# Kernel tuning notes

Measured on AMD Instinct MI355X. Metric: run time of the kernel, lower is better.

Reference implementation:

```python
import jax, jax.numpy as jnp
import numpy as np

NUM_NODES = 16384
NUM_EDGES = 131072
NUM_MOLS = 512
H = 256          # hidden_dim
L = 3            # num_hidden_layers
NUM_RBF = 50
CUTOFF = 5.0
IN_DIM = 5
D_IN = IN_DIM + 3  # atom_types + spherical coords


def setup_inputs() -> dict:
    ks = jax.random.split(jax.random.key(0), 32)
    n = lambda k, s: jax.random.normal(k, s, dtype=jnp.float32) * 0.05
    return {
        "atom_types": jax.random.uniform(ks[0], (NUM_NODES, IN_DIM), dtype=jnp.float32),
        "coords_spherical": jax.random.normal(ks[1], (NUM_NODES, 3), dtype=jnp.float32),
        "edge_dist": jax.random.uniform(ks[2], (NUM_EDGES,), dtype=jnp.float32) * CUTOFF,
        "edge_index": jax.random.randint(ks[3], (2, NUM_EDGES), 0, NUM_NODES, dtype=jnp.int32),
        "node2mol": jnp.arange(NUM_NODES, dtype=jnp.int32) // (NUM_NODES // NUM_MOLS),
        "emb_Wm": n(ks[4], (D_IN, H)), "emb_bm": jnp.zeros((H,), jnp.float32),
        "emb_Wp": n(ks[5], (D_IN, H)), "emb_bp": jnp.zeros((H,), jnp.float32),
        "attn_Wqm": n(ks[6], (L, H, H)), "attn_Wkm": n(ks[7], (L, H, H)), "attn_Wvm": n(ks[8], (L, H, H)),
        "attn_Wqp": n(ks[9], (L, H, H)), "attn_Wkp": n(ks[10], (L, H, H)), "attn_Wvp": n(ks[11], (L, H, H)),
        "attn_We": n(ks[12], (L, NUM_RBF)), "attn_be": jnp.zeros((L,), jnp.float32),
        "mp_We": n(ks[13], (L, NUM_RBF, H)), "mp_be": jnp.zeros((L, H), jnp.float32),
        "mp_Wm": n(ks[14], (L, H, H)), "mp_bm": jnp.zeros((L, H), jnp.float32),
        "mp_Wp": n(ks[15], (L, H, H)), "mp_bp": jnp.zeros((L, H), jnp.float32),
        "ln_g": jnp.ones((L, H), jnp.float32), "ln_b": jnp.zeros((L, H), jnp.float32),
        "proj_W": n(ks[16], (H, H)), "proj_b": jnp.zeros((H,), jnp.float32),
        "head_W1": n(ks[17], (2 * H, H)), "head_b1": jnp.zeros((H,), jnp.float32),
        "head_W2": n(ks[18], (H, H // 2)), "head_b2": jnp.zeros((H // 2,), jnp.float32),
        "head_W3": n(ks[19], (H // 2, 1)), "head_b3": jnp.zeros((1,), jnp.float32),
    }


def _seg_softmax(s, seg, n):
    m = jax.ops.segment_max(s, seg, num_segments=n)
    e = jnp.exp(s - m[seg])
    z = jax.ops.segment_sum(e, seg, num_segments=n)
    return e / (z[seg] + 1e-9)


def _layernorm(x, g, b):
    mu = x.mean(-1, keepdims=True)
    v = ((x - mu) ** 2).mean(-1, keepdims=True)
    return (x - mu) * jax.lax.rsqrt(v + 1e-5) * g + b


def _forward(atom_types, coords_spherical, edge_dist,
             emb_Wm, emb_bm, emb_Wp, emb_bp,
             attn_Wqm, attn_Wkm, attn_Wvm, attn_Wqp, attn_Wkp, attn_Wvp, attn_We, attn_be,
             mp_We, mp_be, mp_Wm, mp_bm, mp_Wp, mp_bp,
             ln_g, ln_b, proj_W, proj_b,
             head_W1, head_b1, head_W2, head_b2, head_W3, head_b3,
             edge_index, node2mol):
    src, dst = edge_index[0], edge_index[1]
    N = NUM_NODES

    # --- RBF expansion (Schutt 2018): 50 gaussians on [0, cutoff] * cosine cutoff ---
    centers = jnp.linspace(0.0, CUTOFF, NUM_RBF)
    delta = CUTOFF / NUM_RBF
    env = 0.5 * (jnp.cos(jnp.pi * edge_dist / CUTOFF) + 1.0) * (edge_dist < CUTOFF)
    rbf = jnp.exp(-0.5 * ((edge_dist[:, None] - centers) / delta) ** 2) * env[:, None]  # [E, R]

    # --- Complex polar embedding ---
    x = jnp.concatenate([atom_types, coords_spherical], axis=-1)  # [N, 8]
    mag = jax.nn.softplus(x @ emb_Wm + emb_bm)
    ph = jnp.pi * jnp.tanh(x @ emb_Wp + emb_bp)

    for l in range(L):
        # --- Complex polar attention: |q||k| cos(phi_q - phi_k), edge bias from rbf ---
        qm, km, vm = mag @ attn_Wqm[l], mag @ attn_Wkm[l], mag @ attn_Wvm[l]
        qp, kp, vp = ph @ attn_Wqp[l], ph @ attn_Wkp[l], ph @ attn_Wvp[l]
        score = jnp.sum(qm[dst] * km[src] * jnp.cos(qp[dst] - kp[src]), axis=-1) / jnp.sqrt(float(H))
        score = score + rbf @ attn_We[l] + attn_be[l]          # [E]
        alpha = _seg_softmax(score, dst, N)                    # [E]
        new_mag = jax.ops.segment_sum(alpha[:, None] * vm[src], dst, num_segments=N)
        new_ph = jax.ops.segment_sum(alpha[:, None] * vp[src], dst, num_segments=N)

        # --- Complex message passing gated by RBF profile ---
        gate = jax.nn.silu(rbf @ mp_We[l] + mp_be[l])          # [E, H]
        agg_m = jax.ops.segment_sum(gate * new_mag[src], dst, num_segments=N)
        agg_p = jax.ops.segment_sum(gate * new_ph[src], dst, num_segments=N)
        new_mag = new_mag + agg_m @ mp_Wm[l] + mp_bm[l]
        new_ph = new_ph + agg_p @ mp_Wp[l] + mp_bp[l]

        # --- residual + LayerNorm on magnitude (dropout = identity at eval) ---
        new_mag = new_mag + mag
        new_ph = new_ph + ph
        mag = _layernorm(new_mag, ln_g[l], ln_b[l])
        ph = new_ph

    # --- real projection + dual (mean, sum) pooling per molecule ---
    atom_repr = (mag * jnp.cos(ph)) @ proj_W + proj_b          # [N, H]
    s = jax.ops.segment_sum(atom_repr, node2mol, num_segments=NUM_MOLS)
    cnt = jax.ops.segment_sum(jnp.ones((N, 1), atom_repr.dtype), node2mol, num_segments=NUM_MOLS)
    mol = jnp.concatenate([s / jnp.maximum(cnt, 1.0), s], axis=-1)  # [B, 2H]

    h = jax.nn.silu(mol @ head_W1 + head_b1)
    h = jax.nn.silu(h @ head_W2 + head_b2)
    return h @ head_W3 + head_b3                               # [B, 1]


def reference(atom_types, coords_spherical, edge_dist,
              emb_Wm, emb_bm, emb_Wp, emb_bp,
              attn_Wqm, attn_Wkm, attn_Wvm, attn_Wqp, attn_Wkp, attn_Wvp, attn_We, attn_be,
              mp_We, mp_be, mp_Wm, mp_bm, mp_Wp, mp_bp,
              ln_g, ln_b, proj_W, proj_b,
              head_W1, head_b1, head_W2, head_b2, head_W3, head_b3,
              edge_index, node2mol):
    return _forward(atom_types, coords_spherical, edge_dist,
                    emb_Wm, emb_bm, emb_Wp, emb_bp,
                    attn_Wqm, attn_Wkm, attn_Wvm, attn_Wqp, attn_Wkp, attn_Wvp, attn_We, attn_be,
                    mp_We, mp_be, mp_Wm, mp_bm, mp_Wp, mp_bp,
                    ln_g, ln_b, proj_W, proj_b,
                    head_W1, head_b1, head_W2, head_b2, head_W3, head_b3,
                    edge_index, node2mol)
```

## Files before the change

### kernel.cpp

```cpp
#include <hip/hip_runtime.h>
#include <math.h>

#define N_NODES 16384
#define N_EDGES 131072
#define N_MOLS 512
#define HDIM 256
#define NLAYER 3
#define NRBF 50
#define CUT 5.0f
#define HH (HDIM*HDIM)

typedef unsigned short u16;
typedef __attribute__((ext_vector_type(8))) short short8v;
typedef __attribute__((ext_vector_type(4))) float f32x4;
typedef __attribute__((ext_vector_type(4))) unsigned short u16x4;

__device__ __forceinline__ float softplusf(float x){ return fmaxf(x,0.f)+log1pf(expf(-fabsf(x))); }
__device__ __forceinline__ float siluf(float x){ return x/(1.f+expf(-x)); }
__device__ __forceinline__ float bf2f(u16 u){ union{unsigned int i; float f;}v; v.i=((unsigned int)u)<<16; return v.f; }
__device__ __forceinline__ u16 f2bf(float f){ union{float f; unsigned int i;}v; v.f=f; unsigned int r = v.i + 0x7FFFu + ((v.i>>16)&1u); return (u16)(r>>16); }

__device__ __forceinline__ void gload_lds16(const void* g, void* l){
  __builtin_amdgcn_global_load_lds((const __attribute__((address_space(1))) unsigned int*)g,
                                   (__attribute__((address_space(3))) unsigned int*)l, 16, 0, 0);
}

__global__ void k_hist(const int* __restrict__ dst, int* __restrict__ cnt){
  int e = blockIdx.x*256 + threadIdx.x;
  if(e < N_EDGES) atomicAdd(&cnt[dst[e]], 1);
}

__global__ __launch_bounds__(1024) void k_scan(const int* __restrict__ cnt,
                                               int* __restrict__ rowptr,
                                               int* __restrict__ cursor){
  __shared__ int part[1024];
  int tid = threadIdx.x;
  int base = tid*16;
  int loc[16]; int s=0;
  #pragma unroll
  for(int i=0;i<16;i++){ loc[i]=s; s+=cnt[base+i]; }
  part[tid]=s; __syncthreads();
  for(int off=1; off<1024; off<<=1){
    int v = (tid>=off)? part[tid-off] : 0;
    __syncthreads();
    part[tid] += v;
    __syncthreads();
  }
  int pre = (tid==0)?0:part[tid-1];
  #pragma unroll
  for(int i=0;i<16;i++){ int v = pre+loc[i]; rowptr[base+i]=v; cursor[base+i]=v; }
  if(tid==1023) rowptr[N_NODES]=part[1023];
}

__global__ void k_scatter(const int* __restrict__ dst, int* __restrict__ cursor,
                          int* __restrict__ perm){
  int e = blockIdx.x*256+threadIdx.x;
  if(e<N_EDGES){ int p = atomicAdd(&cursor[dst[e]],1); perm[p]=e; }
}

__global__ void k_rbf(const float* __restrict__ dist, u16* __restrict__ rbf){
  int gid = blockIdx.x*256+threadIdx.x;
  int e = gid>>6, r = gid&63;
  u16 o = 0;
  if(r<NRBF){
    float d = dist[e];
    float env = 0.5f*(cosf(3.14159265358979f*d/CUT)+1.f) * (d<CUT ? 1.f:0.f);
    float c = CUT*(float)r/(float)(NRBF-1);
    float u = (d - c)/(CUT/(float)NRBF);
    o = f2bf(expf(-0.5f*u*u)*env);
  }
  rbf[(size_t)e*64+r] = o;
}

struct WDesc { const float* src; u16* dst; int K; int dK; };
struct WArgs { WDesc d[28]; };
__global__ __launch_bounds__(256) void k_wconv(WArgs a){
  WDesc w = a.d[blockIdx.x];
  int t = blockIdx.y;
  int ky = t >> 3, nx = t & 7;
  if(ky*32 >= w.dK) return;
  __shared__ float tile[32][33];
  int tid = threadIdx.x;
  int kk = tid >> 3, n4 = (tid & 7)*4;
  int k = ky*32 + kk;
  float4 v = {0.f,0.f,0.f,0.f};
  if(k < w.K) v = *(const float4*)(w.src + (size_t)k*HDIM + nx*32 + n4);
  tile[kk][n4+0]=v.x; tile[kk][n4+1]=v.y; tile[kk][n4+2]=v.z; tile[kk][n4+3]=v.w;
  __syncthreads();
  int nn = tid >> 3, k4 = (tid & 7)*4;
  u16x4 o;
  #pragma unroll
  for(int j=0;j<4;j++) o[j] = f2bf(tile[k4+j][nn]);
  *(u16x4*)(w.dst + (size_t)(nx*32+nn)*w.dK + ky*32 + k4) = o;
}

__global__ void k_embed(const float* __restrict__ at, const float* __restrict__ co,
                        const float* __restrict__ Wm, const float* __restrict__ bm,
                        const float* __restrict__ Wp, const float* __restrict__ bp,
                        float* __restrict__ mag, float* __restrict__ ph,
                        u16* __restrict__ magb, u16* __restrict__ phb){
  int n = blockIdx.x; int h = threadIdx.x;
  __shared__ float x[8];
  if(threadIdx.x<5) x[threadIdx.x] = at[n*5+threadIdx.x];
  else if(threadIdx.x<8) x[threadIdx.x] = co[n*3+threadIdx.x-5];
  __syncthreads();
  float tm=bm[h], tp=bp[h];
  #pragma unroll
  for(int i=0;i<8;i++){ tm = fmaf(x[i],Wm[i*HDIM+h],tm); tp = fmaf(x[i],Wp[i*HDIM+h],tp); }
  size_t idx = (size_t)n*HDIM+h;
  float m = softplusf(tm);
  float p = 3.14159265358979f*tanhf(tp);
  mag[idx]=m; ph[idx]=p; magb[idx]=f2bf(m); phb[idx]=f2bf(p);
}

template<int MODE>
__device__ __forceinline__ void gemm_body(const u16* __restrict__ A,
                                          const u16* __restrict__ Bt,
                                          const float* __restrict__ bias,
                                          void* __restrict__ outp, int K){
  __shared__ __align__(16) u16 As[128*64];
  __shared__ __align__(16) u16 Bs[64*64];
  int tid = threadIdx.x;
  int lane = tid & 63, wid = tid >> 6;
  int wm = wid & 1, wn = wid >> 1;
  int m0 = blockIdx.y * 128;
  int n0 = blockIdx.x * 64;
  const size_t Kb = (size_t)K*2;
  f32x4 acc[4][2] = {};
  for(int k0=0; k0<K; k0+=64){
    #pragma unroll
    for(int it=0; it<4; it++){
      int off = it*4096 + tid*16;
      int row = off >> 7, col = off & 127;
      const char* g = (const char*)A + (size_t)(m0+row)*Kb + (size_t)k0*2 + col;
      gload_lds16(g, (char*)As + it*4096 + wid*1024);
    }
    #pragma unroll
    for(int it=0; it<2; it++){
      int off = it*4096 + tid*16;
      int row = off >> 7, col = off & 127;
      const char* g = (const char*)Bt + (size_t)(n0+row)*Kb + (size_t)k0*2 + col;
      gload_lds16(g, (char*)Bs + it*4096 + wid*1024);
    }
    __syncthreads();
    #pragma unroll
    for(int ks=0; ks<2; ks++){
      int kl = ks*32 + (lane>>4)*8;
      short8v a[4], b[2];
      #pragma unroll
      for(int fm=0; fm<4; fm++){
        int m = wm*64 + fm*16 + (lane&15);
        a[fm] = *(const short8v*)&As[m*64 + kl];
      }
      #pragma unroll
      for(int fn=0; fn<2; fn++){
        int n = wn*32 + fn*16 + (lane&15);
        b[fn] = *(const short8v*)&Bs[n*64 + kl];
      }
      #pragma unroll
      for(int fm=0; fm<4; fm++)
        #pragma unroll
        for(int fn=0; fn<2; fn++)
          acc[fm][fn] = __builtin_amdgcn_mfma_f32_16x16x32_bf16(a[fm], b[fn], acc[fm][fn], 0,0,0);
    }
    __syncthreads();
  }
  int ro = (lane>>4)*4, co = lane&15;
  #pragma unroll
  for(int fm=0; fm<4; fm++){
    #pragma unroll
    for(int fn=0; fn<2; fn++){
      int col = n0 + wn*32 + fn*16 + co;
      float bv = (MODE!=0) ? bias[col] : 0.f;
      #pragma unroll
      for(int r=0; r<4; r++){
        int row = m0 + wm*64 + fm*16 + ro + r;
        float v = acc[fm][fn][r] + bv;
        size_t ci = (size_t)row*HDIM + col;
        if(MODE==0) ((u16*)outp)[ci] = f2bf(v);
        else if(MODE==1) ((u16*)outp)[ci] = f2bf(siluf(v));
        else if(MODE==2) ((float*)outp)[ci] += v;
        else ((float*)outp)[ci] = v;
      }
    }
  }
}

struct QkvArgs { const u16* Wt[6]; u16* out[6]; };
__global__ __launch_bounds__(256,2) void k_gemm_qkv(const u16* __restrict__ magb,
                                                    const u16* __restrict__ phb, QkvArgs q){
  int z = blockIdx.z;
  const u16* A = (z<3) ? magb : phb;
  gemm_body<0>(A, q.Wt[z], nullptr, q.out[z], HDIM);
}
__global__ __launch_bounds__(256,2) void k_gemm_gate(const u16* __restrict__ rbfb,
                                                     const u16* __restrict__ Wt,
                                                     const float* __restrict__ be,
                                                     u16* __restrict__ gate){
  gemm_body<1>(rbfb, Wt, be, gate, 64);
}
struct MpArgs { const u16* A[2]; const u16* Wt[2]; const float* b[2]; float* C[2]; };
__global__ __launch_bounds__(256,2) void k_gemm_mp(MpArgs a){
  int z = blockIdx.z;
  gemm_body<2>(a.A[z], a.Wt[z], a.b[z], a.C[z], HDIM);
}
__global__ __launch_bounds__(256,2) void k_gemm_proj(const u16* __restrict__ Ab,
                                                     const u16* __restrict__ Wt,
                                                     const float* __restrict__ b,
                                                     float* __restrict__ C){
  gemm_body<3>(Ab, Wt, b, C, HDIM);
}

__global__ __launch_bounds__(256) void k_attn_fused(
    const int* __restrict__ rowptr, const int* __restrict__ perm,
    const int* __restrict__ src,
    const u16* __restrict__ qm, const u16* __restrict__ km,
    const u16* __restrict__ qp, const u16* __restrict__ kp,
    const u16* __restrict__ vm, const u16* __restrict__ vp,
    const u16* __restrict__ rbf, const float* __restrict__ We,
    const float* __restrict__ be,
    float* __restrict__ nmag, float* __restrict__ nph,
    u16* __restrict__ nmagb, u16* __restrict__ nphb)
{
  int wid = threadIdx.x >> 6, lane = threadIdx.x & 63;
  int d = blockIdx.x*4 + wid;
  int b = rowptr[d], e = rowptr[d+1];
  size_t qoff = (size_t)d*HDIM + lane*4;
  u16x4 qmv = *(const u16x4*)(qm + qoff);
  u16x4 qpv = *(const u16x4*)(qp + qoff);
  float qm4[4], qp4[4];
  #pragma unroll
  for(int j=0;j<4;j++){ qm4[j]=bf2f(qmv[j]); qp4[j]=bf2f(qpv[j]); }
  float Wel = (lane<NRBF) ? We[lane] : 0.f;
  float be0 = be[0];
  float m = -3.4e38f, z = 0.f;
  float avm[4] = {0.f,0.f,0.f,0.f}, avp[4] = {0.f,0.f,0.f,0.f};
  for(int i=b;i<e;i++){
    int ed = perm[i]; int s = src[ed];
    size_t ko = (size_t)s*HDIM + lane*4;
    u16x4 kmv = *(const u16x4*)(km + ko);
    u16x4 kpv = *(const u16x4*)(kp + ko);
    u16x4 vmv = *(const u16x4*)(vm + ko);
    u16x4 vpv = *(const u16x4*)(vp + ko);
    float rb = (lane<NRBF) ? bf2f(rbf[(size_t)ed*64+lane]) : 0.f;
    float p = 0.f;
    #pragma unroll
    for(int j=0;j<4;j++)
      p = fmaf(qm4[j]*bf2f(kmv[j]), __cosf(qp4[j]-bf2f(kpv[j])), p);
    p = fmaf(rb, Wel, p*0.0625f);
    #pragma unroll
    for(int off=32; off; off>>=1) p += __shfl_xor(p, off, 64);
    float sc = p + be0;
    float mn = fmaxf(m, sc);
    float scale = __expf(m - mn);
    float w = __expf(sc - mn);
    z = fmaf(z, scale, w);
    #pragma unroll
    for(int j=0;j<4;j++){
      avm[j] = fmaf(avm[j], scale, w*bf2f(vmv[j]));
      avp[j] = fmaf(avp[j], scale, w*bf2f(vpv[j]));
    }
    m = mn;
  }
  float inv = 1.f/(z + 1e-9f);
  float4 om, op; u16x4 omb, opb;
  float vo[4], po[4];
  #pragma unroll
  for(int j=0;j<4;j++){ vo[j]=avm[j]*inv; po[j]=avp[j]*inv; omb[j]=f2bf(vo[j]); opb[j]=f2bf(po[j]); }
  om.x=vo[0]; om.y=vo[1]; om.z=vo[2]; om.w=vo[3];
  op.x=po[0]; op.y=po[1]; op.z=po[2]; op.w=po[3];
  *(float4*)(nmag + qoff) = om;
  *(float4*)(nph + qoff) = op;
  *(u16x4*)(nmagb + qoff) = omb;
  *(u16x4*)(nphb + qoff) = opb;
}

__global__ __launch_bounds__(256) void k_mp_agg(const int* __restrict__ rowptr, const int* __restrict__ perm,
                         const int* __restrict__ src, const u16* __restrict__ gate,
                         const u16* __restrict__ nmagb, const u16* __restrict__ nphb,
                         u16* __restrict__ aggm, u16* __restrict__ aggp){
  int wid = threadIdx.x >> 6, lane = threadIdx.x & 63;
  int n = blockIdx.x*4 + wid;
  int b = rowptr[n], e = rowptr[n+1];
  float am[4]={0.f,0.f,0.f,0.f}, ap[4]={0.f,0.f,0.f,0.f};
  for(int i=b;i<e;i++){
    int ed = perm[i]; int s = src[ed];
    u16x4 gv = *(const u16x4*)(gate + (size_t)ed*HDIM + lane*4);
    u16x4 mv = *(const u16x4*)(nmagb + (size_t)s*HDIM + lane*4);
    u16x4 pv = *(const u16x4*)(nphb + (size_t)s*HDIM + lane*4);
    #pragma unroll
    for(int j=0;j<4;j++){
      float g = bf2f(gv[j]);
      am[j] = fmaf(g, bf2f(mv[j]), am[j]);
      ap[j] = fmaf(g, bf2f(pv[j]), ap[j]);
    }
  }
  u16x4 amb, apb;
  #pragma unroll
  for(int j=0;j<4;j++){ amb[j]=f2bf(am[j]); apb[j]=f2bf(ap[j]); }
  size_t o = (size_t)n*HDIM + lane*4;
  *(u16x4*)(aggm + o) = amb;
  *(u16x4*)(aggp + o) = apb;
}

__global__ __launch_bounds__(256) void k_resid_ln(const float* __restrict__ nmag, const float* __restrict__ nph,
                           float* __restrict__ mag, float* __restrict__ ph,
                           u16* __restrict__ magb, u16* __restrict__ phb,
                           const float* __restrict__ g, const float* __restrict__ b){
  int n = blockIdx.x, tid = threadIdx.x;
  size_t idx = (size_t)n*HDIM+tid;
  float t = nmag[idx] + mag[idx];
  float s1=t, s2=t*t;
  #pragma unroll
  for(int off=32; off; off>>=1){ s1 += __shfl_down(s1,off,64); s2 += __shfl_down(s2,off,64); }
  __shared__ float w1[4], w2[4], bc[2];
  int wid = tid>>6, lane = tid&63;
  if(lane==0){ w1[wid]=s1; w2[wid]=s2; }
  __syncthreads();
  if(tid==0){
    float a=w1[0]+w1[1]+w1[2]+w1[3];
    float q=w2[0]+w2[1]+w2[2]+w2[3];
    float mu = a*(1.f/HDIM);
    float var = q*(1.f/HDIM) - mu*mu;
    bc[0]=mu; bc[1]=rsqrtf(var+1e-5f);
  }
  __syncthreads();
  float mu=bc[0], rs=bc[1];
  float ln = (t-mu)*rs*g[tid]+b[tid];
  mag[idx] = ln; magb[idx] = f2bf(ln);
  float p2 = nph[idx] + ph[idx];
  ph[idx] = p2; phb[idx] = f2bf(p2);
}

__global__ void k_tcos(const float* __restrict__ mag, const float* __restrict__ ph,
                       u16* __restrict__ t){
  size_t i = (size_t)blockIdx.x*256+threadIdx.x;
  t[i] = f2bf(mag[i]*cosf(ph[i]));
}

__global__ void k_pool(const float* __restrict__ arepr, const int* __restrict__ n2m,
                       float* __restrict__ spool, float* __restrict__ cntf){
  int gid = blockIdx.x*256+threadIdx.x;
  int n = gid>>8, h = gid&255;
  int m = n2m[n];
  atomicAdd(&spool[(size_t)m*HDIM+h], arepr[(size_t)n*HDIM+h]);
  if(h==0) atomicAdd(&cntf[m], 1.f);
}

__global__ __launch_bounds__(256) void k_head(const float* __restrict__ spool, const float* __restrict__ cntf,
                       const float* __restrict__ W1, const float* __restrict__ b1,
                       const float* __restrict__ W2, const float* __restrict__ b2,
                       const float* __restrict__ W3, const float* __restrict__ b3,
                       float* __restrict__ out){
  __shared__ float smol[2*HDIM];
  __shared__ float sh1[HDIM];
  __shared__ float sh2[HDIM/2];
  int m = blockIdx.x, tid = threadIdx.x;
  float sv = spool[(size_t)m*HDIM+tid];
  float c = cntf[m];
  smol[tid] = sv/fmaxf(c,1.f);
  smol[HDIM+tid] = sv;
  __syncthreads();
  float a = b1[tid];
  for(int i=0;i<2*HDIM;i++) a = fmaf(smol[i], W1[i*HDIM+tid], a);
  sh1[tid] = siluf(a);
  __syncthreads();
  if(tid<128){
    float a2 = b2[tid];
    for(int i=0;i<HDIM;i++) a2 = fmaf(sh1[i], W2[i*128+tid], a2);
    sh2[tid] = siluf(a2);
  }
  __syncthreads();
  if(tid<64){
    float p = sh2[tid]*W3[tid] + sh2[tid+64]*W3[tid+64];
    #pragma unroll
    for(int off=32; off; off>>=1) p += __shfl_down(p,off,64);
    if(tid==0) out[m] = p + b3[0];
  }
}

extern "C" void kernel_launch(void* const* d_in, const int* in_sizes, int n_in,
                              void* d_out, int out_size, void* d_ws, size_t ws_size,
                              hipStream_t stream){
  const float* atom_types = (const float*)d_in[0];
  const float* coords     = (const float*)d_in[1];
  const float* edge_dist  = (const float*)d_in[2];
  const int*   edge_index = (const int*)d_in[3];
  const int*   node2mol   = (const int*)d_in[4];
  const float* emb_Wm = (const float*)d_in[5];
  const float* emb_bm = (const float*)d_in[6];
  const float* emb_Wp = (const float*)d_in[7];
  const float* emb_bp = (const float*)d_in[8];
  const float* attn_Wqm = (const float*)d_in[9];
  const float* attn_Wkm = (const float*)d_in[10];
  const float* attn_Wvm = (const float*)d_in[11];
  const float* attn_Wqp = (const float*)d_in[12];
  const float* attn_Wkp = (const float*)d_in[13];
  const float* attn_Wvp = (const float*)d_in[14];
  const float* attn_We  = (const float*)d_in[15];
  const float* attn_be  = (const float*)d_in[16];
  const float* mp_We = (const float*)d_in[17];
  const float* mp_be = (const float*)d_in[18];
  const float* mp_Wm = (const float*)d_in[19];
  const float* mp_bm = (const float*)d_in[20];
  const float* mp_Wp = (const float*)d_in[21];
  const float* mp_bp = (const float*)d_in[22];
  const float* ln_g = (const float*)d_in[23];
  const float* ln_b = (const float*)d_in[24];
  const float* proj_W = (const float*)d_in[25];
  const float* proj_b = (const float*)d_in[26];
  const float* head_W1 = (const float*)d_in[27];
  const float* head_b1 = (const float*)d_in[28];
  const float* head_W2 = (const float*)d_in[29];
  const float* head_b2 = (const float*)d_in[30];
  const float* head_W3 = (const float*)d_in[31];
  const float* head_b3 = (const float*)d_in[32];
  float* out = (float*)d_out;

  float* ws = (float*)d_ws;
  const size_t NH = (size_t)N_NODES*HDIM;
  size_t o = 0;
  float* mag = ws + o; o += NH;
  float* ph  = ws + o; o += NH;
  float* nmag= ws + o; o += NH;
  float* nph = ws + o; o += NH;
  float* spool = ws + o; o += (size_t)N_MOLS*HDIM;
  float* cntf  = ws + o; o += N_MOLS;
  int* rowptr = (int*)(ws + o); o += N_NODES+1;
  int* cnt    = (int*)(ws + o); o += N_NODES;
  int* cursor = (int*)(ws + o); o += N_NODES;
  int* perm   = (int*)(ws + o); o += N_EDGES + 1;
  u16* magb = (u16*)(ws + o); o += NH/2;
  u16* phb  = (u16*)(ws + o); o += NH/2;
  u16* aggmb= (u16*)(ws + o); o += NH/2;
  u16* aggpb= (u16*)(ws + o); o += NH/2;
  u16* nmagb= (u16*)(ws + o); o += NH/2;
  u16* nphb = (u16*)(ws + o); o += NH/2;
  u16* rbfb = (u16*)(ws + o); o += (size_t)N_EDGES*32;
  u16* arena= (u16*)(ws + o); o += (size_t)N_EDGES*128;
  u16* wt   = (u16*)(ws + o); o += (25*(size_t)HH + 3*HDIM*64)/2;
  u16* qmb = arena + 0*NH; u16* kmb = arena + 1*NH; u16* vmb = arena + 2*NH;
  u16* qpb = arena + 3*NH; u16* kpb = arena + 4*NH; u16* vpb = arena + 5*NH;
  u16* gateb = arena;
  float* arepr = nmag;
  u16* tcosb = aggmb;

  const int* src = edge_index;
  const int* dst = edge_index + N_EDGES;

  WArgs wa;
  for(int l=0;l<NLAYER;l++){
    const float* srcs[6] = {attn_Wqm+(size_t)l*HH, attn_Wkm+(size_t)l*HH, attn_Wvm+(size_t)l*HH,
                            attn_Wqp+(size_t)l*HH, attn_Wkp+(size_t)l*HH, attn_Wvp+(size_t)l*HH};
    for(int j=0;j<6;j++){ wa.d[l*6+j] = { srcs[j], wt + (size_t)(l*6+j)*HH, HDIM, HDIM }; }
    wa.d[18+l] = { mp_Wm+(size_t)l*HH, wt + (size_t)(18+l)*HH, HDIM, HDIM };
    wa.d[21+l] = { mp_Wp+(size_t)l*HH, wt + (size_t)(21+l)*HH, HDIM, HDIM };
    wa.d[25+l] = { mp_We+(size_t)l*NRBF*HDIM, wt + (size_t)25*HH + (size_t)l*HDIM*64, NRBF, 64 };
  }
  wa.d[24] = { proj_W, wt + (size_t)24*HH, HDIM, HDIM };

  hipMemsetAsync(cnt, 0, N_NODES*sizeof(int), stream);
  k_hist<<<N_EDGES/256,256,0,stream>>>(dst, cnt);
  k_scan<<<1,1024,0,stream>>>(cnt, rowptr, cursor);
  k_scatter<<<N_EDGES/256,256,0,stream>>>(dst, cursor, perm);
  k_wconv<<<dim3(28,64),256,0,stream>>>(wa);
  k_rbf<<<(N_EDGES*64)/256,256,0,stream>>>(edge_dist, rbfb);
  k_embed<<<N_NODES,256,0,stream>>>(atom_types, coords, emb_Wm, emb_bm, emb_Wp, emb_bp,
                                    mag, ph, magb, phb);

  dim3 gn(HDIM/64, N_NODES/128);
  dim3 ge(HDIM/64, N_EDGES/128);
  for(int l=0;l<NLAYER;l++){
    QkvArgs qa;
    u16* outs[6] = {qmb, kmb, vmb, qpb, kpb, vpb};
    for(int j=0;j<6;j++){ qa.Wt[j] = wt + (size_t)(l*6+j)*HH; qa.out[j] = outs[j]; }
    k_gemm_qkv<<<dim3(4,128,6),256,0,stream>>>(magb, phb, qa);
    k_attn_fused<<<N_NODES/4,256,0,stream>>>(rowptr, perm, src,
                                             qmb, kmb, qpb, kpb, vmb, vpb,
                                             rbfb, attn_We+(size_t)l*NRBF, attn_be+l,
                                             nmag, nph, nmagb, nphb);
    k_gemm_gate<<<ge,256,0,stream>>>(rbfb, wt + (size_t)25*HH + (size_t)l*HDIM*64,
                                     mp_be+(size_t)l*HDIM, gateb);
    k_mp_agg<<<N_NODES/4,256,0,stream>>>(rowptr, perm, src, gateb, nmagb, nphb, aggmb, aggpb);
    MpArgs ma;
    ma.A[0]=aggmb; ma.A[1]=aggpb;
    ma.Wt[0]=wt + (size_t)(18+l)*HH; ma.Wt[1]=wt + (size_t)(21+l)*HH;
    ma.b[0]=mp_bm+(size_t)l*HDIM; ma.b[1]=mp_bp+(size_t)l*HDIM;
    ma.C[0]=nmag; ma.C[1]=nph;
    k_gemm_mp<<<dim3(4,128,2),256,0,stream>>>(ma);
    k_resid_ln<<<N_NODES,256,0,stream>>>(nmag, nph, mag, ph, magb, phb,
                                         ln_g+(size_t)l*HDIM, ln_b+(size_t)l*HDIM);
  }
  k_tcos<<<NH/256,256,0,stream>>>(mag, ph, tcosb);
  k_gemm_proj<<<gn,256,0,stream>>>(tcosb, wt + (size_t)24*HH, proj_b, arepr);
  hipMemsetAsync(spool, 0, ((size_t)N_MOLS*HDIM+N_MOLS)*sizeof(float), stream);
  k_pool<<<NH/256,256,0,stream>>>(arepr, node2mol, spool, cntf);
  k_head<<<N_MOLS,256,0,stream>>>(spool, cntf, head_W1, head_b1, head_W2, head_b2, head_W3, head_b3, out);
}
```

Baseline: 1.002 ms.

## Pack QKV per node, process two edges per wave, fuse tcos into LN

The QKV GEMM now writes Q/K/V for both branches into one node-major record of 1536 bf16 values, and the new magnitude/phase bf16 outputs are packed per node as well. The attention and aggregation kernels split each wave into two half-waves that handle alternate edges with 8-element vector loads, then combine the halves with a cross-lane shuffle. This is meant to improve gather locality and memory-level parallelism on these memory-bound kernels. Attention drops the running max in its online softmax, which saves the rescaling work but can overflow if scores grow large. The cos-projection prep is fused into the last residual/LayerNorm kernel, which removes one separate kernel and its memory pass.

```diff
diff --git a/kernel.cpp b/kernel.cpp
--- a/kernel.cpp
+++ b/kernel.cpp
@@ -14,6 +14,8 @@
 typedef __attribute__((ext_vector_type(8))) short short8v;
 typedef __attribute__((ext_vector_type(4))) float f32x4;
 typedef __attribute__((ext_vector_type(4))) unsigned short u16x4;
+typedef __attribute__((ext_vector_type(8))) unsigned short u16x8;
+typedef __attribute__((ext_vector_type(2))) unsigned short u16x2;
 
 __device__ __forceinline__ float softplusf(float x){ return fmaxf(x,0.f)+log1pf(expf(-fabsf(x))); }
 __device__ __forceinline__ float siluf(float x){ return x/(1.f+expf(-x)); }
@@ -117,7 +119,7 @@
 __device__ __forceinline__ void gemm_body(const u16* __restrict__ A,
                                           const u16* __restrict__ Bt,
                                           const float* __restrict__ bias,
-                                          void* __restrict__ outp, int K){
+                                          void* __restrict__ outp, int K, int ostr){
   __shared__ __align__(16) u16 As[128*64];
   __shared__ __align__(16) u16 Bs[64*64];
   int tid = threadIdx.x;
@@ -176,7 +178,7 @@
       for(int r=0; r<4; r++){
         int row = m0 + wm*64 + fm*16 + ro + r;
         float v = acc[fm][fn][r] + bv;
-        size_t ci = (size_t)row*HDIM + col;
+        size_t ci = (size_t)row*ostr + col;
         if(MODE==0) ((u16*)outp)[ci] = f2bf(v);
         else if(MODE==1) ((u16*)outp)[ci] = f2bf(siluf(v));
         else if(MODE==2) ((float*)outp)[ci] += v;
@@ -191,121 +193,136 @@
                                                     const u16* __restrict__ phb, QkvArgs q){
   int z = blockIdx.z;
   const u16* A = (z<3) ? magb : phb;
-  gemm_body<0>(A, q.Wt[z], nullptr, q.out[z], HDIM);
+  gemm_body<0>(A, q.Wt[z], nullptr, q.out[z], HDIM, 1536);
 }
 __global__ __launch_bounds__(256,2) void k_gemm_gate(const u16* __restrict__ rbfb,
                                                      const u16* __restrict__ Wt,
                                                      const float* __restrict__ be,
                                                      u16* __restrict__ gate){
-  gemm_body<1>(rbfb, Wt, be, gate, 64);
+  gemm_body<1>(rbfb, Wt, be, gate, 64, 256);
 }
 struct MpArgs { const u16* A[2]; const u16* Wt[2]; const float* b[2]; float* C[2]; };
 __global__ __launch_bounds__(256,2) void k_gemm_mp(MpArgs a){
   int z = blockIdx.z;
-  gemm_body<2>(a.A[z], a.Wt[z], a.b[z], a.C[z], HDIM);
+  gemm_body<2>(a.A[z], a.Wt[z], a.b[z], a.C[z], HDIM, 256);
 }
 __global__ __launch_bounds__(256,2) void k_gemm_proj(const u16* __restrict__ Ab,
                                                      const u16* __restrict__ Wt,
                                                      const float* __restrict__ b,
                                                      float* __restrict__ C){
-  gemm_body<3>(Ab, Wt, b, C, HDIM);
+  gemm_body<3>(Ab, Wt, b, C, HDIM, 256);
 }
 
 __global__ __launch_bounds__(256) void k_attn_fused(
     const int* __restrict__ rowptr, const int* __restrict__ perm,
     const int* __restrict__ src,
-    const u16* __restrict__ qm, const u16* __restrict__ km,
-    const u16* __restrict__ qp, const u16* __restrict__ kp,
-    const u16* __restrict__ vm, const u16* __restrict__ vp,
-    const u16* __restrict__ rbf, const float* __restrict__ We,
-    const float* __restrict__ be,
+    const u16* __restrict__ pack, const u16* __restrict__ rbf,
+    const float* __restrict__ We, const float* __restrict__ be,
     float* __restrict__ nmag, float* __restrict__ nph,
-    u16* __restrict__ nmagb, u16* __restrict__ nphb)
+    u16* __restrict__ npack)
 {
   int wid = threadIdx.x >> 6, lane = threadIdx.x & 63;
+  int hid = lane >> 5, l = lane & 31;
   int d = blockIdx.x*4 + wid;
   int b = rowptr[d], e = rowptr[d+1];
-  size_t qoff = (size_t)d*HDIM + lane*4;
-  u16x4 qmv = *(const u16x4*)(qm + qoff);
-  u16x4 qpv = *(const u16x4*)(qp + qoff);
-  float qm4[4], qp4[4];
-  #pragma unroll
-  for(int j=0;j<4;j++){ qm4[j]=bf2f(qmv[j]); qp4[j]=bf2f(qpv[j]); }
-  float Wel = (lane<NRBF) ? We[lane] : 0.f;
+  const u16* qb = pack + (size_t)d*1536 + l*8;
+  u16x8 qm8 = *(const u16x8*)qb;
+  u16x8 qp8 = *(const u16x8*)(qb + 256);
+  float qmf[8], qpf[8];
+  #pragma unroll
+  for(int j=0;j<8;j++){ qmf[j]=bf2f(qm8[j]); qpf[j]=bf2f(qp8[j]); }
+  float We0 = (2*l   < NRBF) ? We[2*l]   : 0.f;
+  float We1 = (2*l+1 < NRBF) ? We[2*l+1] : 0.f;
   float be0 = be[0];
-  float m = -3.4e38f, z = 0.f;
-  float avm[4] = {0.f,0.f,0.f,0.f}, avp[4] = {0.f,0.f,0.f,0.f};
-  for(int i=b;i<e;i++){
+  float z = 0.f;
+  float avm[8] = {0,0,0,0,0,0,0,0}, avp[8] = {0,0,0,0,0,0,0,0};
+  for(int i = b + hid; i < e; i += 2){
     int ed = perm[i]; int s = src[ed];
-    size_t ko = (size_t)s*HDIM + lane*4;
-    u16x4 kmv = *(const u16x4*)(km + ko);
-    u16x4 kpv = *(const u16x4*)(kp + ko);
-    u16x4 vmv = *(const u16x4*)(vm + ko);
-    u16x4 vpv = *(const u16x4*)(vp + ko);
-    float rb = (lane<NRBF) ? bf2f(rbf[(size_t)ed*64+lane]) : 0.f;
+    const u16* kb = pack + (size_t)s*1536 + l*8;
+    u16x8 km8 = *(const u16x8*)(kb + 512);
+    u16x8 kp8 = *(const u16x8*)(kb + 768);
+    u16x8 vm8 = *(const u16x8*)(kb + 1024);
+    u16x8 vp8 = *(const u16x8*)(kb + 1280);
+    u16x2 rb2 = *(const u16x2*)(rbf + (size_t)ed*64 + 2*l);
     float p = 0.f;
     #pragma unroll
-    for(int j=0;j<4;j++)
-      p = fmaf(qm4[j]*bf2f(kmv[j]), __cosf(qp4[j]-bf2f(kpv[j])), p);
-    p = fmaf(rb, Wel, p*0.0625f);
-    #pragma unroll
-    for(int off=32; off; off>>=1) p += __shfl_xor(p, off, 64);
-    float sc = p + be0;
-    float mn = fmaxf(m, sc);
-    float scale = __expf(m - mn);
-    float w = __expf(sc - mn);
-    z = fmaf(z, scale, w);
-    #pragma unroll
-    for(int j=0;j<4;j++){
-      avm[j] = fmaf(avm[j], scale, w*bf2f(vmv[j]));
-      avp[j] = fmaf(avp[j], scale, w*bf2f(vpv[j]));
+    for(int j=0;j<8;j++)
+      p = fmaf(qmf[j]*bf2f(km8[j]), __cosf(qpf[j]-bf2f(kp8[j])), p);
+    float t = fmaf(bf2f(rb2[0]), We0, fmaf(bf2f(rb2[1]), We1, p*0.0625f));
+    #pragma unroll
+    for(int off=16; off; off>>=1) t += __shfl_xor(t, off, 64);
+    float w = __expf(t + be0);
+    z += w;
+    #pragma unroll
+    for(int j=0;j<8;j++){
+      avm[j] = fmaf(w, bf2f(vm8[j]), avm[j]);
+      avp[j] = fmaf(w, bf2f(vp8[j]), avp[j]);
     }
-    m = mn;
-  }
-  float inv = 1.f/(z + 1e-9f);
-  float4 om, op; u16x4 omb, opb;
-  float vo[4], po[4];
-  #pragma unroll
-  for(int j=0;j<4;j++){ vo[j]=avm[j]*inv; po[j]=avp[j]*inv; omb[j]=f2bf(vo[j]); opb[j]=f2bf(po[j]); }
-  om.x=vo[0]; om.y=vo[1]; om.z=vo[2]; om.w=vo[3];
-  op.x=po[0]; op.y=po[1]; op.z=po[2]; op.w=po[3];
-  *(float4*)(nmag + qoff) = om;
-  *(float4*)(nph + qoff) = op;
-  *(u16x4*)(nmagb + qoff) = omb;
-  *(u16x4*)(nphb + qoff) = opb;
+  }
+  z += __shfl_xor(z, 32, 64);
+  #pragma unroll
+  for(int j=0;j<8;j++){
+    avm[j] += __shfl_xor(avm[j], 32, 64);
+    avp[j] += __shfl_xor(avp[j], 32, 64);
+  }
+  if(hid==0){
+    float inv = 1.f/(z + 1e-9f);
+    u16x8 mb, pb;
+    #pragma unroll
+    for(int j=0;j<8;j++){ avm[j]*=inv; avp[j]*=inv; mb[j]=f2bf(avm[j]); pb[j]=f2bf(avp[j]); }
+    size_t no = (size_t)d*256 + l*8;
+    *(float4*)(nmag + no)     = make_float4(avm[0],avm[1],avm[2],avm[3]);
+    *(float4*)(nmag + no + 4) = make_float4(avm[4],avm[5],avm[6],avm[7]);
+    *(float4*)(nph + no)      = make_float4(avp[0],avp[1],avp[2],avp[3]);
+    *(float4*)(nph + no + 4)  = make_float4(avp[4],avp[5],avp[6],avp[7]);
+    u16* nb = npack + (size_t)d*512 + l*8;
+    *(u16x8*)nb = mb;
+    *(u16x8*)(nb + 256) = pb;
+  }
 }
 
 __global__ __launch_bounds__(256) void k_mp_agg(const int* __restrict__ rowptr, const int* __restrict__ perm,
                          const int* __restrict__ src, const u16* __restrict__ gate,
-                         const u16* __restrict__ nmagb, const u16* __restrict__ nphb,
+                         const u16* __restrict__ npack,
                          u16* __restrict__ aggm, u16* __restrict__ aggp){
   int wid = threadIdx.x >> 6, lane = threadIdx.x & 63;
+  int hid = lane >> 5, l = lane & 31;
   int n = blockIdx.x*4 + wid;
   int b = rowptr[n], e = rowptr[n+1];
-  float am[4]={0.f,0.f,0.f,0.f}, ap[4]={0.f,0.f,0.f,0.f};
-  for(int i=b;i<e;i++){
+  float am[8] = {0,0,0,0,0,0,0,0}, ap[8] = {0,0,0,0,0,0,0,0};
+  for(int i = b + hid; i < e; i += 2){
     int ed = perm[i]; int s = src[ed];
-    u16x4 gv = *(const u16x4*)(gate + (size_t)ed*HDIM + lane*4);
-    u16x4 mv = *(const u16x4*)(nmagb + (size_t)s*HDIM + lane*4);
-    u16x4 pv = *(const u16x4*)(nphb + (size_t)s*HDIM + lane*4);
-    #pragma unroll
-    for(int j=0;j<4;j++){
-      float g = bf2f(gv[j]);
-      am[j] = fmaf(g, bf2f(mv[j]), am[j]);
-      ap[j] = fmaf(g, bf2f(pv[j]), ap[j]);
+    u16x8 g8 = *(const u16x8*)(gate + (size_t)ed*256 + l*8);
+    const u16* nb = npack + (size_t)s*512 + l*8;
+    u16x8 m8 = *(const u16x8*)nb;
+    u16x8 p8 = *(const u16x8*)(nb + 256);
+    #pragma unroll
+    for(int j=0;j<8;j++){
+      float g = bf2f(g8[j]);
+      am[j] = fmaf(g, bf2f(m8[j]), am[j]);
+      ap[j] = fmaf(g, bf2f(p8[j]), ap[j]);
     }
   }
-  u16x4 amb, apb;
-  #pragma unroll
-  for(int j=0;j<4;j++){ amb[j]=f2bf(am[j]); apb[j]=f2bf(ap[j]); }
-  size_t o = (size_t)n*HDIM + lane*4;
-  *(u16x4*)(aggm + o) = amb;
-  *(u16x4*)(aggp + o) = apb;
-}
-
+  #pragma unroll
+  for(int j=0;j<8;j++){
+    am[j] += __shfl_xor(am[j], 32, 64);
+    ap[j] += __shfl_xor(ap[j], 32, 64);
+  }
+  if(hid==0){
+    u16x8 amb, apb;
+    #pragma unroll
+    for(int j=0;j<8;j++){ amb[j]=f2bf(am[j]); apb[j]=f2bf(ap[j]); }
+    size_t o = (size_t)n*256 + l*8;
+    *(u16x8*)(aggm + o) = amb;
+    *(u16x8*)(aggp + o) = apb;
+  }
+}
+
+template<int LAST>
 __global__ __launch_bounds__(256) void k_resid_ln(const float* __restrict__ nmag, const float* __restrict__ nph,
                            float* __restrict__ mag, float* __restrict__ ph,
                            u16* __restrict__ magb, u16* __restrict__ phb,
+                           u16* __restrict__ tcosb,
                            const float* __restrict__ g, const float* __restrict__ b){
   int n = blockIdx.x, tid = threadIdx.x;
   size_t idx = (size_t)n*HDIM+tid;
@@ -327,15 +344,13 @@
   __syncthreads();
   float mu=bc[0], rs=bc[1];
   float ln = (t-mu)*rs*g[tid]+b[tid];
-  mag[idx] = ln; magb[idx] = f2bf(ln);
   float p2 = nph[idx] + ph[idx];
-  ph[idx] = p2; phb[idx] = f2bf(p2);
-}
-
-__global__ void k_tcos(const float* __restrict__ mag, const float* __restrict__ ph,
-                       u16* __restrict__ t){
-  size_t i = (size_t)blockIdx.x*256+threadIdx.x;
-  t[i] = f2bf(mag[i]*cosf(ph[i]));
+  if(LAST){
+    tcosb[idx] = f2bf(ln*__cosf(p2));
+  } else {
+    mag[idx] = ln; magb[idx] = f2bf(ln);
+    ph[idx] = p2; phb[idx] = f2bf(p2);
+  }
 }
 
 __global__ void k_pool(const float* __restrict__ arepr, const int* __restrict__ n2m,
@@ -434,13 +449,11 @@
   u16* phb  = (u16*)(ws + o); o += NH/2;
   u16* aggmb= (u16*)(ws + o); o += NH/2;
   u16* aggpb= (u16*)(ws + o); o += NH/2;
-  u16* nmagb= (u16*)(ws + o); o += NH/2;
-  u16* nphb = (u16*)(ws + o); o += NH/2;
+  u16* npack= (u16*)(ws + o); o += NH;
   u16* rbfb = (u16*)(ws + o); o += (size_t)N_EDGES*32;
   u16* arena= (u16*)(ws + o); o += (size_t)N_EDGES*128;
   u16* wt   = (u16*)(ws + o); o += (25*(size_t)HH + 3*HDIM*64)/2;
-  u16* qmb = arena + 0*NH; u16* kmb = arena + 1*NH; u16* vmb = arena + 2*NH;
-  u16* qpb = arena + 3*NH; u16* kpb = arena + 4*NH; u16* vpb = arena + 5*NH;
+  u16* pack = arena;
   u16* gateb = arena;
   float* arepr = nmag;
   u16* tcosb = aggmb;
@@ -472,26 +485,28 @@
   dim3 ge(HDIM/64, N_EDGES/128);
   for(int l=0;l<NLAYER;l++){
     QkvArgs qa;
-    u16* outs[6] = {qmb, kmb, vmb, qpb, kpb, vpb};
-    for(int j=0;j<6;j++){ qa.Wt[j] = wt + (size_t)(l*6+j)*HH; qa.out[j] = outs[j]; }
+    const int zoff[6] = {0, 512, 1024, 256, 768, 1280};
+    for(int j=0;j<6;j++){ qa.Wt[j] = wt + (size_t)(l*6+j)*HH; qa.out[j] = pack + zoff[j]; }
     k_gemm_qkv<<<dim3(4,128,6),256,0,stream>>>(magb, phb, qa);
-    k_attn_fused<<<N_NODES/4,256,0,stream>>>(rowptr, perm, src,
-                                             qmb, kmb, qpb, kpb, vmb, vpb,
+    k_attn_fused<<<N_NODES/4,256,0,stream>>>(rowptr, perm, src, pack,
                                              rbfb, attn_We+(size_t)l*NRBF, attn_be+l,
-                                             nmag, nph, nmagb, nphb);
+                                             nmag, nph, npack);
     k_gemm_gate<<<ge,256,0,stream>>>(rbfb, wt + (size_t)25*HH + (size_t)l*HDIM*64,
                                      mp_be+(size_t)l*HDIM, gateb);
-    k_mp_agg<<<N_NODES/4,256,0,stream>>>(rowptr, perm, src, gateb, nmagb, nphb, aggmb, aggpb);
+    k_mp_agg<<<N_NODES/4,256,0,stream>>>(rowptr, perm, src, gateb, npack, aggmb, aggpb);
     MpArgs ma;
     ma.A[0]=aggmb; ma.A[1]=aggpb;
     ma.Wt[0]=wt + (size_t)(18+l)*HH; ma.Wt[1]=wt + (size_t)(21+l)*HH;
     ma.b[0]=mp_bm+(size_t)l*HDIM; ma.b[1]=mp_bp+(size_t)l*HDIM;
     ma.C[0]=nmag; ma.C[1]=nph;
     k_gemm_mp<<<dim3(4,128,2),256,0,stream>>>(ma);
-    k_resid_ln<<<N_NODES,256,0,stream>>>(nmag, nph, mag, ph, magb, phb,
-                                         ln_g+(size_t)l*HDIM, ln_b+(size_t)l*HDIM);
-  }
-  k_tcos<<<NH/256,256,0,stream>>>(mag, ph, tcosb);
+    if(l < NLAYER-1)
+      k_resid_ln<0><<<N_NODES,256,0,stream>>>(nmag, nph, mag, ph, magb, phb, nullptr,
+                                              ln_g+(size_t)l*HDIM, ln_b+(size_t)l*HDIM);
+    else
+      k_resid_ln<1><<<N_NODES,256,0,stream>>>(nmag, nph, mag, ph, magb, phb, tcosb,
+                                              ln_g+(size_t)l*HDIM, ln_b+(size_t)l*HDIM);
+  }
   k_gemm_proj<<<gn,256,0,stream>>>(tcosb, wt + (size_t)24*HH, proj_b, arepr);
   hipMemsetAsync(spool, 0, ((size_t)N_MOLS*HDIM+N_MOLS)*sizeof(float), stream);
   k_pool<<<NH/256,256,0,stream>>>(arepr, node2mol, spool, cntf);
```

Result: faster. 943.6 us (-5.9%).
